# Kernel optimization log

Hardware: AMD Instinct MI355X
Metric: run time of the kernel (lower is better)

## Reference

```python
import jax, jax.numpy as jnp
import numpy as np

B, C, G, P, W, H = 16, 64, 256, 4096, 1024, 256
WQ = W // 4  # wsi_dim // 4 = 256
D = C + G + WQ  # concat dim fed to score MLP = 576


def _init_linear(key, fan_in, fan_out):
    k1, k2 = jax.random.split(key)
    bound = 1.0 / np.sqrt(fan_in)
    w = jax.random.uniform(k1, (fan_in, fan_out), jnp.float32, -bound, bound)
    b = jax.random.uniform(k2, (fan_out,), jnp.float32, -bound, bound)
    return w, b


def setup_inputs() -> dict:
    key = jax.random.key(0)
    ks = jax.random.split(key, 8)
    cx = jax.random.normal(ks[0], (B, C), jnp.float32)
    gx = jax.random.normal(ks[1], (B, G), jnp.float32)
    wx = jax.random.normal(ks[2], (B, P, W), jnp.float32)
    Wc, bc = _init_linear(ks[3], C, C)        # fc_c
    Wg, bg = _init_linear(ks[4], G, G)        # fc_g
    Ww, bw = _init_linear(ks[5], W, WQ)       # fc_w
    W1, b1 = _init_linear(ks[6], D, H)        # FCLayers hidden
    W2, b2 = _init_linear(ks[7], H, 1)        # FCLayers out
    return {"cx": cx, "gx": gx, "wx": wx,
            "Wc": Wc, "bc": bc, "Wg": Wg, "bg": bg, "Ww": Ww, "bw": bw,
            "W1": W1, "b1": b1, "W2": W2, "b2": b2}


def reference(cx, gx, wx, Wc, bc, Wg, bg, Ww, bw, W1, b1, W2, b2):
    # Per-modality projections
    c = cx @ Wc + bc                      # [B, C]
    g = gx @ Wg + bg                      # [B, G]
    w = jnp.einsum('bpw,wq->bpq', wx, Ww) + bw  # [B, P, WQ]
    # Score MLP on concat(c, g, w_i) for every patch, vectorized by
    # splitting W1 rows over the concat blocks (avoids materializing concat):
    W1c, W1g, W1w = W1[:C], W1[C:C + G], W1[C + G:]
    h = jax.nn.relu((c @ W1c + g @ W1g + b1)[:, None, :]
                    + jnp.einsum('bpq,qh->bph', w, W1w))  # [B, P, H]
    scores = h @ W2 + b2                  # [B, P, 1]
    attn = jax.nn.softmax(scores, axis=1)  # softmax over patches
    return jnp.sum(attn * w, axis=1)      # [B, WQ]
```

## Files before the change

### kernel.cpp

```cpp
#include <hip/hip_runtime.h>
#include <hip/hip_bf16.h>

#define B_   16
#define C_   64
#define G_   256
#define P_   4096
#define W_   1024
#define H_   256
#define WQ_  256
#define M_   (B_ * P_)

typedef __attribute__((ext_vector_type(8))) _Float16 f16x8;
typedef __attribute__((ext_vector_type(4))) float    f32x4;

__device__ __forceinline__ float h2f(ushort u) {
    union { ushort u; _Float16 h; } cv; cv.u = u;
    return (float)cv.h;
}

#define GLOAD16(gsrc, ldst)                                                  \
    __builtin_amdgcn_global_load_lds(                                        \
        (const __attribute__((address_space(1))) unsigned int*)(gsrc),       \
        (__attribute__((address_space(3))) unsigned int*)(ldst), 16, 0, 0)

__device__ __forceinline__ int inv_swz64(int o) {
    const int b8 = (o >> 8) & 1, b7 = (o >> 7) & 1, b6 = (o >> 6) & 1;
    const int b5 = (o >> 5) & 1, b4 = (o >> 4) & 1;
    const int l6 = b6 ^ b8, l5 = b5 ^ b7, l4 = b4 ^ l6;
    return (o & ~0x70) | (l6 << 6) | (l5 << 5) | (l4 << 4);
}

__device__ __forceinline__ void convT_dev(
    const float* __restrict__ src, ushort* __restrict__ dst,
    int K, int N, int blk, float* tile )
{
    const int nb = N >> 6;
    const int k0 = (blk / nb) * 64;
    const int n0 = (blk % nb) * 64;
    const int t = threadIdx.x;
    #pragma unroll
    for (int i = 0; i < 16; ++i) {
        int e = i * 256 + t;
        int kr = e >> 6, nc = e & 63;
        tile[nc * 65 + kr] = src[(size_t)(k0 + kr) * N + n0 + nc];
    }
    __syncthreads();
    #pragma unroll
    for (int i = 0; i < 16; ++i) {
        int e = i * 256 + t;
        int nc = e >> 6, kr = e & 63;
        union { _Float16 h; ushort u; } cv;
        cv.h = (_Float16)tile[nc * 65 + kr];
        dst[(size_t)(n0 + nc) * K + k0 + kr] = cv.u;
    }
}

__global__ __launch_bounds__(256) void setup_kernel(
    const float* __restrict__ Ww,  ushort* __restrict__ WwT,
    const float* __restrict__ W1w, ushort* __restrict__ W1T,
    const float* __restrict__ cx, const float* __restrict__ gx,
    const float* __restrict__ Wc, const float* __restrict__ bc,
    const float* __restrict__ Wg, const float* __restrict__ bg,
    const float* __restrict__ W1, const float* __restrict__ b1,
    float* __restrict__ base_out)
{
    __shared__ float smem[64 * 65];
    const int blk = blockIdx.x;
    if (blk < 64) {
        convT_dev(Ww, WwT, W_, WQ_, blk, smem);
        return;
    }
    if (blk < 80) {
        convT_dev(W1w, W1T, H_, H_, blk - 64, smem);
        return;
    }
    const int b = blk - 80;
    const int t = threadIdx.x;
    float* cxl = smem;
    float* gxl = smem + 64;
    float* cl  = smem + 320;
    float* gl  = smem + 384;

    if (t < C_) cxl[t] = cx[b * C_ + t];
    gxl[t] = gx[b * G_ + t];
    __syncthreads();

    if (t < C_) {
        float acc = bc[t];
        #pragma unroll 4
        for (int i = 0; i < C_; ++i) acc += cxl[i] * Wc[i * C_ + t];
        cl[t] = acc;
    }
    {
        float acc = bg[t];
        #pragma unroll 4
        for (int i = 0; i < G_; ++i) acc += gxl[i] * Wg[i * G_ + t];
        gl[t] = acc;
    }
    __syncthreads();

    float acc = b1[t];
    #pragma unroll 4
    for (int i = 0; i < C_; ++i) acc += cl[i] * W1[i * H_ + t];
    #pragma unroll 4
    for (int i = 0; i < G_; ++i) acc += gl[i] * W1[(C_ + i) * H_ + t];
    base_out[b * H_ + t] = acc;
}

__global__ __launch_bounds__(512, 2) void gemm_w_fused(
    const float* __restrict__ A,
    const ushort* __restrict__ BT,
    const float* __restrict__ bw,
    const ushort* __restrict__ W1T,
    const float* __restrict__ base_,
    const float* __restrict__ W2,
    const float* __restrict__ b2,
    ushort* Cout,
    float* __restrict__ scores)
{
    __shared__ __align__(16) char smem[65536];
    ushort* wt = (ushort*)smem;

    const int t = threadIdx.x;
    const int row0 = blockIdx.x * 128;
    const int b = blockIdx.x >> 5;
    const int lane = t & 63, wave = t >> 6;
    const int wm = wave >> 2, wn = wave & 3;
    const int l15 = lane & 15, lq = lane >> 4;

    const int oA0 = t * 16, oA1 = t * 16 + 8192;
    const int rA0 = oA0 >> 7, rA1 = oA1 >> 7;
    const float* srcA0 = A + (size_t)(row0 + rA0) * W_
                           + (((oA0 & 127) ^ ((rA0 & 7) << 4)) >> 2);
    const float* srcA1 = A + (size_t)(row0 + rA1) * W_
                           + (((oA1 & 127) ^ ((rA1 & 7) << 4)) >> 2);
    const int oB0 = t * 16, oB1 = t * 16 + 8192;
    const int lB0 = inv_swz64(oB0), lB1 = inv_swz64(oB1);
    const ushort* srcB0 = BT + (size_t)(lB0 >> 6) * W_ + ((lB0 & 63) >> 1);
    const ushort* srcB1 = BT + (size_t)(lB1 >> 6) * W_ + ((lB1 & 63) >> 1);

#define STAGE1(BUF, K0)                                                      \
    {                                                                        \
        char* ab = smem + (BUF) * 16384;                                     \
        char* bb = smem + 32768 + (BUF) * 16384;                             \
        GLOAD16(srcA0 + (K0), ab + oA0);                                     \
        GLOAD16(srcA1 + (K0), ab + oA1);                                     \
        GLOAD16(srcB0 + (K0), bb + oB0);                                     \
        GLOAD16(srcB1 + (K0), bb + oB1);                                     \
    }

    f32x4 acc[4][4];
    #pragma unroll
    for (int m = 0; m < 4; ++m)
        #pragma unroll
        for (int n = 0; n < 4; ++n) acc[m][n] = (f32x4){0.f, 0.f, 0.f, 0.f};

    STAGE1(0, 0)
    __syncthreads();

    for (int kt = 0; kt < 32; ++kt) {
        const int cur = kt & 1;
        if (kt + 1 < 32) STAGE1(cur ^ 1, (kt + 1) * 32)
        const char* Af = smem + cur * 16384;
        const char* Bh = smem + 32768 + cur * 16384;

        f16x8 af[4], bf[4];
        #pragma unroll
        for (int m = 0; m < 4; ++m) {
            const int r = wm * 64 + m * 16 + l15;
            const int g = r * 128 + lq * 32;
            const int swz = (r & 7) << 4;
            const f32x4 a0 = *(const f32x4*)(Af + (g ^ swz));
            const f32x4 a1 = *(const f32x4*)(Af + ((g + 16) ^ swz));
            f16x8 h;
            h[0] = (_Float16)a0[0]; h[1] = (_Float16)a0[1];
            h[2] = (_Float16)a0[2]; h[3] = (_Float16)a0[3];
            h[4] = (_Float16)a1[0]; h[5] = (_Float16)a1[1];
            h[6] = (_Float16)a1[2]; h[7] = (_Float16)a1[3];
            af[m] = h;
        }
        #pragma unroll
        for (int n = 0; n < 4; ++n) {
            const int c = wn * 64 + n * 16 + l15;
            const int byte = (c * 64 + lq * 16) ^ ((c & 7) << 4);
            bf[n] = *(const f16x8*)(Bh + byte);
        }
        #pragma unroll
        for (int m = 0; m < 4; ++m)
            #pragma unroll
            for (int n = 0; n < 4; ++n)
                acc[m][n] = __builtin_amdgcn_mfma_f32_16x16x32_f16(
                    af[m], bf[n], acc[m][n], 0, 0, 0);
        __syncthreads();
    }
#undef STAGE1

    {
        float bwv[4];
        #pragma unroll
        for (int n = 0; n < 4; ++n) bwv[n] = bw[wn * 64 + n * 16 + l15];
        #pragma unroll
        for (int m = 0; m < 4; ++m)
            #pragma unroll
            for (int reg = 0; reg < 4; ++reg) {
                const int rl = wm * 64 + m * 16 + lq * 4 + reg;
                #pragma unroll
                for (int n = 0; n < 4; ++n) {
                    const int col = wn * 64 + n * 16 + l15;
                    union { _Float16 h; ushort u; } cv;
                    cv.h = (_Float16)(acc[m][n][reg] + bwv[n]);
                    Cout[(size_t)(row0 + rl) * WQ_ + col] = cv.u;
                    *(ushort*)((char*)wt + ((rl * 512 + col * 2) ^ ((rl & 7) << 4))) = cv.u;
                }
            }
    }
    __syncthreads();

    f32x4 acc2[4][4];
    #pragma unroll
    for (int m = 0; m < 4; ++m)
        #pragma unroll
        for (int n = 0; n < 4; ++n) acc2[m][n] = (f32x4){0.f, 0.f, 0.f, 0.f};

    for (int k2 = 0; k2 < WQ_; k2 += 32) {
        f16x8 af[4], bf[4];
        #pragma unroll
        for (int m = 0; m < 4; ++m) {
            const int r = wm * 64 + m * 16 + l15;
            const int byte = (r * 512 + (k2 + lq * 8) * 2) ^ ((r & 7) << 4);
            af[m] = *(const f16x8*)((const char*)wt + byte);
        }
        #pragma unroll
        for (int n = 0; n < 4; ++n) {
            const int c = wn * 64 + n * 16 + l15;
            bf[n] = *(const f16x8*)(W1T + (size_t)c * WQ_ + k2 + lq * 8);
        }
        #pragma unroll
        for (int m = 0; m < 4; ++m)
            #pragma unroll
            for (int n = 0; n < 4; ++n)
                acc2[m][n] = __builtin_amdgcn_mfma_f32_16x16x32_f16(
                    af[m], bf[n], acc2[m][n], 0, 0, 0);
    }

    __syncthreads();
    {
        float (*red2)[128] = (float(*)[128])smem;
        float basev[4], w2v[4];
        #pragma unroll
        for (int n = 0; n < 4; ++n) {
            const int col = wn * 64 + n * 16 + l15;
            basev[n] = base_[b * H_ + col];
            w2v[n] = W2[col];
        }
        #pragma unroll
        for (int m = 0; m < 4; ++m)
            #pragma unroll
            for (int reg = 0; reg < 4; ++reg) {
                float s = 0.f;
                #pragma unroll
                for (int n = 0; n < 4; ++n) {
                    float h = acc2[m][n][reg] + basev[n];
                    h = fmaxf(h, 0.f);
                    s += h * w2v[n];
                }
                s += __shfl_xor(s, 1, 64);
                s += __shfl_xor(s, 2, 64);
                s += __shfl_xor(s, 4, 64);
                s += __shfl_xor(s, 8, 64);
                if (l15 == 0) red2[wn][wm * 64 + m * 16 + lq * 4 + reg] = s;
            }
        __syncthreads();
        if (t < 128) {
            scores[row0 + t] =
                red2[0][t] + red2[1][t] + red2[2][t] + red2[3][t] + b2[0];
        }
    }
}

__global__ __launch_bounds__(256) void weighted_partial_kernel(
    const ushort* __restrict__ wmat16, const float* __restrict__ scores,
    float* __restrict__ part)
{
    const int blk = blockIdx.x;
    const int b   = blk >> 5;
    const int sl  = blk & 31;
    const int t   = threadIdx.x;
    const int rg  = t >> 5;
    const int q8  = (t & 31) * 8;
    __shared__ float red[8][WQ_];
    __shared__ float mred[4];

    float mv = -1e30f;
    for (int p = t; p < P_; p += 256) mv = fmaxf(mv, scores[b * P_ + p]);
    #pragma unroll
    for (int d = 1; d < 64; d <<= 1) mv = fmaxf(mv, __shfl_xor(mv, d, 64));
    if ((t & 63) == 0) mred[t >> 6] = mv;
    __syncthreads();
    const float m = fmaxf(fmaxf(mred[0], mred[1]), fmaxf(mred[2], mred[3]));

    float acc[8];
    #pragma unroll
    for (int j = 0; j < 8; ++j) acc[j] = 0.f;

    const int p0 = sl * 128 + rg * 16;
    for (int p = p0; p < p0 + 16; ++p) {
        const float e = expf(scores[b * P_ + p] - m);
        const uint4 raw = *(const uint4*)(wmat16 + ((size_t)b * P_ + p) * WQ_ + q8);
        const ushort* u = (const ushort*)&raw;
        #pragma unroll
        for (int j = 0; j < 8; ++j) acc[j] += e * h2f(u[j]);
    }
    #pragma unroll
    for (int j = 0; j < 8; ++j) red[rg][q8 + j] = acc[j];
    __syncthreads();
    float s = 0.f;
    #pragma unroll
    for (int g = 0; g < 8; ++g) s += red[g][t];
    part[(size_t)(b * 32 + sl) * WQ_ + t] = s;
}

__global__ __launch_bounds__(256) void finalize_kernel(
    const float* __restrict__ part, const float* __restrict__ scores,
    float* __restrict__ out)
{
    const int b = blockIdx.x;
    const int t = threadIdx.x;
    __shared__ float mred[4];
    __shared__ float zred[4];

    float mv = -1e30f;
    for (int p = t; p < P_; p += 256) mv = fmaxf(mv, scores[b * P_ + p]);
    #pragma unroll
    for (int d = 1; d < 64; d <<= 1) mv = fmaxf(mv, __shfl_xor(mv, d, 64));
    if ((t & 63) == 0) mred[t >> 6] = mv;
    __syncthreads();
    const float m = fmaxf(fmaxf(mred[0], mred[1]), fmaxf(mred[2], mred[3]));

    float zv = 0.f;
    for (int p = t; p < P_; p += 256) zv += expf(scores[b * P_ + p] - m);
    #pragma unroll
    for (int d = 1; d < 64; d <<= 1) zv += __shfl_xor(zv, d, 64);
    if ((t & 63) == 0) zred[t >> 6] = zv;
    __syncthreads();
    const float z = zred[0] + zred[1] + zred[2] + zred[3];

    float acc = 0.f;
    #pragma unroll
    for (int sl = 0; sl < 32; ++sl) acc += part[(size_t)(b * 32 + sl) * WQ_ + t];
    out[b * WQ_ + t] = acc / z;
}

extern "C" void kernel_launch(void* const* d_in, const int* in_sizes, int n_in,
                              void* d_out, int out_size, void* d_ws, size_t ws_size,
                              hipStream_t stream) {
    const float* cx = (const float*)d_in[0];
    const float* gx = (const float*)d_in[1];
    const float* wx = (const float*)d_in[2];
    const float* Wc = (const float*)d_in[3];
    const float* bc = (const float*)d_in[4];
    const float* Wg = (const float*)d_in[5];
    const float* bg = (const float*)d_in[6];
    const float* Ww = (const float*)d_in[7];
    const float* bw = (const float*)d_in[8];
    const float* W1 = (const float*)d_in[9];
    const float* b1 = (const float*)d_in[10];
    const float* W2 = (const float*)d_in[11];
    const float* b2 = (const float*)d_in[12];
    float* out = (float*)d_out;

    float* ws        = (float*)d_ws;
    ushort* ws_w16   = (ushort*)ws;
    float* ws_scores = ws + (size_t)M_ * WQ_ / 2;
    float* ws_base   = ws_scores + M_;
    float* ws_part   = ws_base + B_ * H_;
    ushort* WwT16    = (ushort*)(ws_part + B_ * 32 * WQ_);
    ushort* W1T16    = WwT16 + (size_t)W_ * WQ_;

    setup_kernel<<<96, 256, 0, stream>>>(
        Ww, WwT16, W1 + (size_t)(C_ + G_) * H_, W1T16,
        cx, gx, Wc, bc, Wg, bg, W1, b1, ws_base);

    gemm_w_fused<<<M_ / 128, 512, 0, stream>>>(
        wx, WwT16, bw, W1T16, ws_base, W2, b2, ws_w16, ws_scores);

    weighted_partial_kernel<<<B_ * 32, 256, 0, stream>>>(ws_w16, ws_scores, ws_part);

    finalize_kernel<<<B_, 256, 0, stream>>>(ws_part, ws_scores, out);
}
```

Baseline: 183.5 us.

## Halve fused GEMM row tile, pre-convert A to fp16 in LDS, raise occupancy

The fused projection+MLP kernel now processes 64 rows per block instead of 128, doubling the grid. The wx tile is loaded through registers and converted to fp16 before it is written to LDS, instead of being staged as fp32 with global_load_lds and converted at fragment-read time. This shrinks LDS from 64 KB to 40 KB and moves the reduction buffer to a non-overlapping region, which lets one barrier be dropped. The launch bound is raised so more blocks can share a CU, with the aim of hiding latency. The risks are register pressure or spills from the tight occupancy target, and the loss of the asynchronous direct-to-LDS load for A.

```diff
diff --git a/kernel.cpp b/kernel.cpp
--- a/kernel.cpp
+++ b/kernel.cpp
@@ -107,7 +107,7 @@
     base_out[b * H_ + t] = acc;
 }
 
-__global__ __launch_bounds__(512, 2) void gemm_w_fused(
+__global__ __launch_bounds__(512, 6) void gemm_w_fused(
     const float* __restrict__ A,
     const ushort* __restrict__ BT,
     const float* __restrict__ bw,
@@ -118,92 +118,88 @@
     ushort* Cout,
     float* __restrict__ scores)
 {
-    __shared__ __align__(16) char smem[65536];
+    __shared__ __align__(16) char smem[40960];
     ushort* wt = (ushort*)smem;
+    float (*red2)[64] = (float(*)[64])(smem + 32768);
 
     const int t = threadIdx.x;
-    const int row0 = blockIdx.x * 128;
-    const int b = blockIdx.x >> 5;
+    const int row0 = blockIdx.x * 64;
+    const int b = blockIdx.x >> 6;
     const int lane = t & 63, wave = t >> 6;
     const int wm = wave >> 2, wn = wave & 3;
     const int l15 = lane & 15, lq = lane >> 4;
 
-    const int oA0 = t * 16, oA1 = t * 16 + 8192;
-    const int rA0 = oA0 >> 7, rA1 = oA1 >> 7;
-    const float* srcA0 = A + (size_t)(row0 + rA0) * W_
-                           + (((oA0 & 127) ^ ((rA0 & 7) << 4)) >> 2);
-    const float* srcA1 = A + (size_t)(row0 + rA1) * W_
-                           + (((oA1 & 127) ^ ((rA1 & 7) << 4)) >> 2);
+    const int a_r = t >> 2, a_g = t & 3;
+    const int a_dst = (a_r * 64 + a_g * 16) ^ ((a_r & 7) << 4);
+    const float* a_src = A + (size_t)(row0 + a_r) * W_ + a_g * 8;
     const int oB0 = t * 16, oB1 = t * 16 + 8192;
     const int lB0 = inv_swz64(oB0), lB1 = inv_swz64(oB1);
     const ushort* srcB0 = BT + (size_t)(lB0 >> 6) * W_ + ((lB0 & 63) >> 1);
     const ushort* srcB1 = BT + (size_t)(lB1 >> 6) * W_ + ((lB1 & 63) >> 1);
 
-#define STAGE1(BUF, K0)                                                      \
+#define STAGE(BUF, K0)                                                       \
     {                                                                        \
-        char* ab = smem + (BUF) * 16384;                                     \
-        char* bb = smem + 32768 + (BUF) * 16384;                             \
-        GLOAD16(srcA0 + (K0), ab + oA0);                                     \
-        GLOAD16(srcA1 + (K0), ab + oA1);                                     \
+        char* bb = smem + 8192 + (BUF) * 16384;                              \
         GLOAD16(srcB0 + (K0), bb + oB0);                                     \
         GLOAD16(srcB1 + (K0), bb + oB1);                                     \
-    }
-
-    f32x4 acc[4][4];
-    #pragma unroll
-    for (int m = 0; m < 4; ++m)
+        if (t < 256) {                                                       \
+            char* ab = smem + (BUF) * 4096;                                  \
+            const float4 v0 = *(const float4*)(a_src + (K0));                \
+            const float4 v1 = *(const float4*)(a_src + (K0) + 4);            \
+            f16x8 h;                                                         \
+            h[0] = (_Float16)v0.x; h[1] = (_Float16)v0.y;                    \
+            h[2] = (_Float16)v0.z; h[3] = (_Float16)v0.w;                    \
+            h[4] = (_Float16)v1.x; h[5] = (_Float16)v1.y;                    \
+            h[6] = (_Float16)v1.z; h[7] = (_Float16)v1.w;                    \
+            *(f16x8*)(ab + a_dst) = h;                                       \
+        }                                                                    \
+    }
+
+    f32x4 acc[2][4];
+    #pragma unroll
+    for (int m = 0; m < 2; ++m)
         #pragma unroll
         for (int n = 0; n < 4; ++n) acc[m][n] = (f32x4){0.f, 0.f, 0.f, 0.f};
 
-    STAGE1(0, 0)
+    STAGE(0, 0)
     __syncthreads();
 
     for (int kt = 0; kt < 32; ++kt) {
         const int cur = kt & 1;
-        if (kt + 1 < 32) STAGE1(cur ^ 1, (kt + 1) * 32)
-        const char* Af = smem + cur * 16384;
-        const char* Bh = smem + 32768 + cur * 16384;
-
-        f16x8 af[4], bf[4];
-        #pragma unroll
-        for (int m = 0; m < 4; ++m) {
-            const int r = wm * 64 + m * 16 + l15;
-            const int g = r * 128 + lq * 32;
-            const int swz = (r & 7) << 4;
-            const f32x4 a0 = *(const f32x4*)(Af + (g ^ swz));
-            const f32x4 a1 = *(const f32x4*)(Af + ((g + 16) ^ swz));
-            f16x8 h;
-            h[0] = (_Float16)a0[0]; h[1] = (_Float16)a0[1];
-            h[2] = (_Float16)a0[2]; h[3] = (_Float16)a0[3];
-            h[4] = (_Float16)a1[0]; h[5] = (_Float16)a1[1];
-            h[6] = (_Float16)a1[2]; h[7] = (_Float16)a1[3];
-            af[m] = h;
+        if (kt + 1 < 32) STAGE(cur ^ 1, (kt + 1) * 32)
+        const char* Ah = smem + cur * 4096;
+        const char* Bh = smem + 8192 + cur * 16384;
+
+        f16x8 af[2], bf[4];
+        #pragma unroll
+        for (int m = 0; m < 2; ++m) {
+            const int r = wm * 32 + m * 16 + l15;
+            af[m] = *(const f16x8*)(Ah + ((r * 64 + lq * 16) ^ ((r & 7) << 4)));
         }
         #pragma unroll
         for (int n = 0; n < 4; ++n) {
             const int c = wn * 64 + n * 16 + l15;
-            const int byte = (c * 64 + lq * 16) ^ ((c & 7) << 4);
-            bf[n] = *(const f16x8*)(Bh + byte);
-        }
-        #pragma unroll
-        for (int m = 0; m < 4; ++m)
+            bf[n] = *(const f16x8*)(Bh + ((c * 64 + lq * 16) ^ ((c & 7) << 4)));
+        }
+        #pragma unroll
+        for (int m = 0; m < 2; ++m)
             #pragma unroll
             for (int n = 0; n < 4; ++n)
                 acc[m][n] = __builtin_amdgcn_mfma_f32_16x16x32_f16(
                     af[m], bf[n], acc[m][n], 0, 0, 0);
         __syncthreads();
     }
-#undef STAGE1
+#undef STAGE
 
     {
         float bwv[4];
         #pragma unroll
         for (int n = 0; n < 4; ++n) bwv[n] = bw[wn * 64 + n * 16 + l15];
         #pragma unroll
-        for (int m = 0; m < 4; ++m)
+        for (int m = 0; m < 2; ++m)
             #pragma unroll
             for (int reg = 0; reg < 4; ++reg) {
-                const int rl = wm * 64 + m * 16 + lq * 4 + reg;
+                const int rl = wm * 32 + m * 16 + lq * 4 + reg;
                 #pragma unroll
                 for (int n = 0; n < 4; ++n) {
                     const int col = wn * 64 + n * 16 + l15;
@@ -216,17 +212,17 @@
     }
     __syncthreads();
 
-    f32x4 acc2[4][4];
-    #pragma unroll
-    for (int m = 0; m < 4; ++m)
+    f32x4 acc2[2][4];
+    #pragma unroll
+    for (int m = 0; m < 2; ++m)
         #pragma unroll
         for (int n = 0; n < 4; ++n) acc2[m][n] = (f32x4){0.f, 0.f, 0.f, 0.f};
 
     for (int k2 = 0; k2 < WQ_; k2 += 32) {
-        f16x8 af[4], bf[4];
-        #pragma unroll
-        for (int m = 0; m < 4; ++m) {
-            const int r = wm * 64 + m * 16 + l15;
+        f16x8 af[2], bf[4];
+        #pragma unroll
+        for (int m = 0; m < 2; ++m) {
+            const int r = wm * 32 + m * 16 + l15;
             const int byte = (r * 512 + (k2 + lq * 8) * 2) ^ ((r & 7) << 4);
             af[m] = *(const f16x8*)((const char*)wt + byte);
         }
@@ -236,16 +232,14 @@
             bf[n] = *(const f16x8*)(W1T + (size_t)c * WQ_ + k2 + lq * 8);
         }
         #pragma unroll
-        for (int m = 0; m < 4; ++m)
+        for (int m = 0; m < 2; ++m)
             #pragma unroll
             for (int n = 0; n < 4; ++n)
                 acc2[m][n] = __builtin_amdgcn_mfma_f32_16x16x32_f16(
                     af[m], bf[n], acc2[m][n], 0, 0, 0);
     }
 
-    __syncthreads();
     {
-        float (*red2)[128] = (float(*)[128])smem;
         float basev[4], w2v[4];
         #pragma unroll
         for (int n = 0; n < 4; ++n) {
@@ -254,7 +248,7 @@
             w2v[n] = W2[col];
         }
         #pragma unroll
-        for (int m = 0; m < 4; ++m)
+        for (int m = 0; m < 2; ++m)
             #pragma unroll
             for (int reg = 0; reg < 4; ++reg) {
                 float s = 0.f;
@@ -268,10 +262,10 @@
                 s += __shfl_xor(s, 2, 64);
                 s += __shfl_xor(s, 4, 64);
                 s += __shfl_xor(s, 8, 64);
-                if (l15 == 0) red2[wn][wm * 64 + m * 16 + lq * 4 + reg] = s;
+                if (l15 == 0) red2[wn][wm * 32 + m * 16 + lq * 4 + reg] = s;
             }
         __syncthreads();
-        if (t < 128) {
+        if (t < 64) {
             scores[row0 + t] =
                 red2[0][t] + red2[1][t] + red2[2][t] + red2[3][t] + b2[0];
         }
@@ -381,7 +375,7 @@
         Ww, WwT16, W1 + (size_t)(C_ + G_) * H_, W1T16,
         cx, gx, Wc, bc, Wg, bg, W1, b1, ws_base);
 
-    gemm_w_fused<<<M_ / 128, 512, 0, stream>>>(
+    gemm_w_fused<<<M_ / 64, 512, 0, stream>>>(
         wx, WwT16, bw, W1T16, ws_base, W2, b2, ws_w16, ws_scores);
 
     weighted_partial_kernel<<<B_ * 32, 256, 0, stream>>>(ws_w16, ws_scores, ws_part);
```

Result: slower. 201.3 us (+9.7%).
